# Optimization experiments

Measured on AMD Instinct MI355X. Metric: run time of the kernel, lower is better.

The kernel has to match this reference:

```python
import jax, jax.numpy as jnp
import numpy as np

N_GROUPS = 8
TOPK_GROUPS = 4
TOPK = 8
ROUTE_SCALE = 2.5

def setup_inputs() -> dict:
    key = jax.random.key(0)
    k1, k2, k3 = jax.random.split(key, 3)
    B, D, E = 8192, 7168, 256
    x = jax.random.normal(k1, (B, D), dtype=jnp.float32)
    weight = jax.random.normal(k2, (E, D), dtype=jnp.float32) / np.sqrt(D)
    bias = jax.random.normal(k3, (E,), dtype=jnp.float32) * 0.01
    return {"x": x, "weight": weight, "bias": bias}

def reference(x, weight, bias):
    B = x.shape[0]
    # linear scores: (B, E)
    scores = jnp.einsum('bd,ed->be', x, weight)
    # sigmoid score function
    s = jax.nn.sigmoid(scores)
    original_scores = s
    # bias correction for group selection (bias is not None since dim==7168)
    sb = s + bias
    # group view: (B, G, E/G)
    sg = sb.reshape(B, N_GROUPS, -1)
    # group score = sum of top-2 per group (bias branch)
    group_scores = jax.lax.top_k(sg, 2)[0].sum(axis=-1)  # (B, G)
    gidx = jax.lax.top_k(group_scores, TOPK_GROUPS)[1]   # (B, topk_groups)
    # boolean mask of selected groups
    gmask = jnp.zeros((B, N_GROUPS), dtype=bool).at[jnp.arange(B)[:, None], gidx].set(True)
    sg = jnp.where(gmask[:, :, None], sg, -jnp.inf)
    flat = sg.reshape(B, -1)  # (B, E)
    indices = jax.lax.top_k(flat, TOPK)[1]               # (B, topk)
    weights = jnp.take_along_axis(original_scores, indices, axis=1)
    # sigmoid path: normalize to sum 1, then scale
    weights = weights / weights.sum(axis=-1, keepdims=True)
    weights = weights * ROUTE_SCALE
    return weights.astype(x.dtype), indices
```

## Files before the change

kernel.cpp:

```cpp
#include <hip/hip_runtime.h>
#include <hip/hip_bf16.h>
#include <math.h>

#define DDIM 7168
#define NEXP 256
#define NGRP 8
#define TOPKG 4
#define TOPK 8
#define ROUTE_SCALE 2.5f

#define BM 128
#define BN 256
#define BK 32
#define KSPLIT 4
#define KPER (DDIM / KSPLIT)
#define NSTEP (KPER / BK)
#define NKTILE (DDIM / BK)
#define BT_ELEMS (NEXP * BK * 2)
#define AT_FLOATS (BM * BK)

typedef __attribute__((ext_vector_type(8))) short bf16x8;
typedef __attribute__((ext_vector_type(4))) float f32x4;
typedef unsigned int u32;
typedef unsigned short ushort_t;

static __device__ __forceinline__ ushort_t bf16_rne(float f) {
    u32 b = __float_as_uint(f);
    u32 r = (b + 0x7fffu + ((b >> 16) & 1u)) >> 16;
    return (ushort_t)r;
}
static __device__ __forceinline__ float bf16_to_f32(ushort_t h) {
    return __uint_as_float(((u32)h) << 16);
}
static __device__ __forceinline__ void split_elem(float f, short& h, short& l) {
    union { __hip_bfloat16 b; short s; } cv;
    cv.b = __float2bfloat16(f);
    h = cv.s;
    float hf = __uint_as_float(((u32)(ushort_t)cv.s) << 16);
    cv.b = __float2bfloat16(f - hf);
    l = cv.s;
}

__global__ __launch_bounds__(256) void wsplit_kernel(const float* __restrict__ w,
                                                     short* __restrict__ wsp)
{
    const int kt = blockIdx.x;
    const int e  = threadIdx.x;
    const float* wp = w + (size_t)e * DDIM + (size_t)kt * BK;
    short* tb = wsp + (size_t)kt * BT_ELEMS;
    const int fn = e >> 4, er = e & 15;
    #pragma unroll
    for (int jg = 0; jg < 4; jg++) {
        float f[8];
        *(float4*)&f[0] = *(const float4*)(wp + jg * 8);
        *(float4*)&f[4] = *(const float4*)(wp + jg * 8 + 4);
        ushort_t h[8], l[8];
        #pragma unroll
        for (int j = 0; j < 8; j++) {
            h[j] = bf16_rne(f[j]);
            l[j] = bf16_rne(f[j] - bf16_to_f32(h[j]));
        }
        const int lane = jg * 16 + er;
        *(uint4*)(tb + ((size_t)(0 * 16 + fn) * 64 + lane) * 8) = *(uint4*)h;
        *(uint4*)(tb + ((size_t)(1 * 16 + fn) * 64 + lane) * 8) = *(uint4*)l;
    }
}

__global__ __launch_bounds__(512, 2) void gemm_split_kernel(
    const float* __restrict__ x, const short* __restrict__ wsp,
    float* __restrict__ part, int Btok)
{
    __shared__ short Blds[3][BT_ELEMS];
    __shared__ float Alds[3][AT_FLOATS];

    const int bid  = blockIdx.x;
    const int xcd  = bid & 7;
    const int ksp  = xcd & 3;
    const int mt   = (bid >> 3) * 2 + (xcd >> 2);
    const int m0   = mt * BM;
    const int kbase = ksp * KPER;
    const int t    = threadIdx.x;
    const int wid  = t >> 6, lane = t & 63;
    const int wm   = wid >> 2, wn = wid & 3;
    const int lr   = lane & 15, lg = lane >> 4;

    const short* wt0 = wsp + (size_t)(ksp * NSTEP) * BT_ELEMS;

    const int arow0 = wid * 16 + (lane >> 3);
    const int akoff = 4 * ((lane & 7) ^ ((lane >> 3) & 7));
    const float* asrc0 = x + (size_t)(m0 + arow0) * DDIM + kbase + akoff;
    const size_t arow_step = (size_t)8 * DDIM;
    const int adst0 = wid * 2048 + lane * 16;

#define STAGE_B(stp, bptr) do {                                                            \
        const short* gt_ = wt0 + (size_t)(stp) * BT_ELEMS;                                 \
        _Pragma("unroll")                                                                  \
        for (int i_ = 0; i_ < 4; i_++) {                                                   \
            const int off_ = wid * 4096 + i_ * 1024;                                       \
            __builtin_amdgcn_global_load_lds(                                              \
                (const __attribute__((address_space(1))) u32*)((const char*)gt_ + off_ + lane * 16), \
                (__attribute__((address_space(3))) u32*)((char*)(bptr) + off_),            \
                16, 0, 0);                                                                 \
        } } while (0)

#define STAGE_A(stp, aptr) do {                                                            \
        _Pragma("unroll")                                                                  \
        for (int i_ = 0; i_ < 2; i_++) {                                                   \
            __builtin_amdgcn_global_load_lds(                                              \
                (const __attribute__((address_space(1))) u32*)(asrc0 + (size_t)i_ * arow_step + (size_t)(stp) * BK), \
                (__attribute__((address_space(3))) u32*)((char*)(aptr) + adst0 + i_ * 1024), \
                16, 0, 0);                                                                 \
        } } while (0)

    f32x4 acc[4][4];
    #pragma unroll
    for (int i = 0; i < 4; i++)
        #pragma unroll
        for (int j = 0; j < 4; j++) acc[i][j] = (f32x4){0.f, 0.f, 0.f, 0.f};

    short* pB_r = &Blds[0][0]; short* pB_1 = &Blds[1][0]; short* pB_2 = &Blds[2][0];
    float* pA_r = &Alds[0][0]; float* pA_1 = &Alds[1][0]; float* pA_2 = &Alds[2][0];

    STAGE_B(0, pB_r); STAGE_A(0, pA_r);
    STAGE_B(1, pB_1); STAGE_A(1, pA_1);

    for (int st = 0; st < NSTEP; st++) {
        if (st < NSTEP - 1) { asm volatile("s_waitcnt vmcnt(6)" ::: "memory"); }
        else                { asm volatile("s_waitcnt vmcnt(0)" ::: "memory"); }
        asm volatile("s_waitcnt lgkmcnt(0)" ::: "memory");
        __builtin_amdgcn_s_barrier();
        asm volatile("" ::: "memory");

        if (st + 2 < NSTEP) { STAGE_B(st + 2, pB_2); STAGE_A(st + 2, pA_2); }

        const char* ab = (const char*)pA_r;
        bf16x8 ah[4], al[4];
        #pragma unroll
        for (int fm = 0; fm < 4; fm++) {
            const int row = wm * 64 + fm * 16 + lr;
            const int rb  = row * 128;
            const int sw  = (lr & 7) << 4;
            float fr[8];
            *(float4*)&fr[0] = *(const float4*)(ab + rb + ((lg * 32) ^ sw));
            *(float4*)&fr[4] = *(const float4*)(ab + rb + ((lg * 32 + 16) ^ sw));
            union { bf16x8 v; short s[8]; } H, L;
            #pragma unroll
            for (int j = 0; j < 8; j++)
                split_elem(fr[j], H.s[j], L.s[j]);
            ah[fm] = H.v;
            al[fm] = L.v;
        }

        bf16x8 bhv[4], blv[4];
        #pragma unroll
        for (int fn = 0; fn < 4; fn++) {
            bhv[fn] = *(const bf16x8*)&pB_r[((size_t)(0 * 16 + wn * 4 + fn) * 64 + lane) * 8];
            blv[fn] = *(const bf16x8*)&pB_r[((size_t)(1 * 16 + wn * 4 + fn) * 64 + lane) * 8];
        }
        #pragma unroll
        for (int fn = 0; fn < 4; fn++)
            #pragma unroll
            for (int fm = 0; fm < 4; fm++)
                acc[fm][fn] = __builtin_amdgcn_mfma_f32_16x16x32_bf16(ah[fm], bhv[fn], acc[fm][fn], 0, 0, 0);
        #pragma unroll
        for (int fn = 0; fn < 4; fn++)
            #pragma unroll
            for (int fm = 0; fm < 4; fm++)
                acc[fm][fn] = __builtin_amdgcn_mfma_f32_16x16x32_bf16(ah[fm], blv[fn], acc[fm][fn], 0, 0, 0);
        #pragma unroll
        for (int fn = 0; fn < 4; fn++)
            #pragma unroll
            for (int fm = 0; fm < 4; fm++)
                acc[fm][fn] = __builtin_amdgcn_mfma_f32_16x16x32_bf16(al[fm], bhv[fn], acc[fm][fn], 0, 0, 0);

        { short* tb_ = pB_r; pB_r = pB_1; pB_1 = pB_2; pB_2 = tb_; }
        { float* ta_ = pA_r; pA_r = pA_1; pA_1 = pA_2; pA_2 = ta_; }
    }
#undef STAGE_B
#undef STAGE_A

    float* pp = part + (size_t)ksp * (size_t)Btok * NEXP;
    #pragma unroll
    for (int fm = 0; fm < 4; fm++) {
        const int row0 = m0 + wm * 64 + fm * 16 + lg * 4;
        #pragma unroll
        for (int fn = 0; fn < 4; fn++) {
            const int col = wn * 64 + fn * 16 + lr;
            #pragma unroll
            for (int rr = 0; rr < 4; rr++)
                pp[(size_t)(row0 + rr) * NEXP + col] = acc[fm][fn][rr];
        }
    }
}

__global__ __launch_bounds__(256) void gate_kernel(
    const float* __restrict__ part, const float* __restrict__ bias,
    float* __restrict__ out_w, float* __restrict__ out_i, int B)
{
    const int lane = threadIdx.x & 63;
    const int wid  = threadIdx.x >> 6;
    const int row  = blockIdx.x * 4 + wid;
    if (row >= B) return;

    const size_t plane = (size_t)B * NEXP;
    const float* pr = part + (size_t)row * NEXP + lane * 4;
    float4 v0 = *(const float4*)(pr);
    float4 v1 = *(const float4*)(pr + plane);
    float4 v2 = *(const float4*)(pr + 2 * plane);
    float4 v3 = *(const float4*)(pr + 3 * plane);
    float sc[4] = { v0.x + v1.x + v2.x + v3.x,
                    v0.y + v1.y + v2.y + v3.y,
                    v0.z + v1.z + v2.z + v3.z,
                    v0.w + v1.w + v2.w + v3.w };
    float4 bv = *(const float4*)(bias + lane * 4);
    const float bb[4] = { bv.x, bv.y, bv.z, bv.w };

    float so[4], sb[4];
    #pragma unroll
    for (int j = 0; j < 4; j++) {
        so[j] = 1.0f / (1.0f + expf(-sc[j]));
        sb[j] = so[j] + bb[j];
    }

    float m1 = sb[0], m2 = -INFINITY;
    #pragma unroll
    for (int j = 1; j < 4; j++) {
        if (sb[j] > m1)      { m2 = m1; m1 = sb[j]; }
        else if (sb[j] > m2) { m2 = sb[j]; }
    }
    #pragma unroll
    for (int m = 1; m <= 4; m <<= 1) {
        float o1 = __shfl_xor(m1, m);
        float o2 = __shfl_xor(m2, m);
        float hi = fmaxf(m1, o1);
        float lo = fminf(m1, o1);
        m1 = hi;
        m2 = fmaxf(lo, fmaxf(m2, o2));
    }
    float gscore = m1 + m2;
    int g = lane >> 3;

    float gs[NGRP];
    #pragma unroll
    for (int gg = 0; gg < NGRP; gg++) gs[gg] = __shfl(gscore, gg * 8);
    int rank = 0;
    #pragma unroll
    for (int gg = 0; gg < NGRP; gg++) {
        if (gg == g) continue;
        if (gs[gg] > gs[g] || (gs[gg] == gs[g] && gg < g)) rank++;
    }
    const bool selg = (rank < TOPKG);
    float mv[4];
    #pragma unroll
    for (int j = 0; j < 4; j++) mv[j] = selg ? sb[j] : -INFINITY;

    float wsel[TOPK];
    int   isel[TOPK];
    float wsum = 0.f;
    #pragma unroll
    for (int it = 0; it < TOPK; it++) {
        float v = mv[0]; int jj = 0;
        #pragma unroll
        for (int j = 1; j < 4; j++)
            if (mv[j] > v) { v = mv[j]; jj = j; }
        int gi = (lane << 2) | jj;
        #pragma unroll
        for (int m = 1; m < 64; m <<= 1) {
            float ov = __shfl_xor(v, m);
            int   oi = __shfl_xor(gi, m);
            if (ov > v || (ov == v && oi < gi)) { v = ov; gi = oi; }
        }
        int slot = gi & 3, src = gi >> 2;
        float cand = (slot == 0) ? so[0] : (slot == 1) ? so[1] : (slot == 2) ? so[2] : so[3];
        float sval = __shfl(cand, src);
        wsel[it] = sval; isel[it] = gi; wsum += sval;
        if (lane == src) mv[slot] = -INFINITY;
    }

    if (lane == 0) {
        float scl = ROUTE_SCALE / wsum;
        #pragma unroll
        for (int it = 0; it < TOPK; it++) {
            out_w[(size_t)row * TOPK + it] = wsel[it] * scl;
            out_i[(size_t)row * TOPK + it] = (float)isel[it];
        }
    }
}

extern "C" void kernel_launch(void* const* d_in, const int* in_sizes, int n_in,
                              void* d_out, int out_size, void* d_ws, size_t ws_size,
                              hipStream_t stream)
{
    const float* x    = (const float*)d_in[0];
    const float* w    = (const float*)d_in[1];
    const float* bias = (const float*)d_in[2];
    const int B = in_sizes[0] / DDIM;

    float* part = (float*)d_ws;
    short* wsp  = (short*)((char*)d_ws + (size_t)KSPLIT * B * NEXP * sizeof(float));

    float* out_w = (float*)d_out;
    float* out_i = out_w + (size_t)B * TOPK;

    hipLaunchKernelGGL(wsplit_kernel, dim3(NKTILE), dim3(256), 0, stream, w, wsp);
    hipLaunchKernelGGL(gemm_split_kernel, dim3((B / BM) * KSPLIT), dim3(512), 0, stream,
                       x, wsp, part, B);
    hipLaunchKernelGGL(gate_kernel, dim3((B + 3) / 4), dim3(256), 0, stream,
                       part, bias, out_w, out_i, B);
}
```

Baseline: 144.3 us.

## Split GEMM tile along experts into two 128-column halves with double buffering

The gemm block tile shrinks from 128x256 to 128x128, so each block covers half of the experts. The grid doubles and blocks drop from 512 to 256 threads. The pre-split weight layout is reorganized into per-half tiles, and the triple-buffered pipeline with manual waitcnt is replaced by a simpler double buffer using __syncthreads. This cuts LDS per block and raises block count, at the cost of loading each x tile twice (once per expert half) and a shallower prefetch pipeline.

Measured after the change: 141.4 us. 1.02x faster.

```diff
diff --git a/kernel.cpp b/kernel.cpp
--- a/kernel.cpp
+++ b/kernel.cpp
@@ -10,13 +10,13 @@
 #define ROUTE_SCALE 2.5f
 
 #define BM 128
-#define BN 256
+#define BN 128
 #define BK 32
 #define KSPLIT 4
 #define KPER (DDIM / KSPLIT)
 #define NSTEP (KPER / BK)
 #define NKTILE (DDIM / BK)
-#define BT_ELEMS (NEXP * BK * 2)
+#define BT_ELEMS (BN * BK * 2)
 #define AT_FLOATS (BM * BK)
 
 typedef __attribute__((ext_vector_type(8))) short bf16x8;
@@ -47,8 +47,8 @@
     const int kt = blockIdx.x;
     const int e  = threadIdx.x;
     const float* wp = w + (size_t)e * DDIM + (size_t)kt * BK;
-    short* tb = wsp + (size_t)kt * BT_ELEMS;
-    const int fn = e >> 4, er = e & 15;
+    const int nh = e >> 7, fn = (e >> 4) & 7, er = e & 15;
+    short* tb = wsp + ((size_t)kt * 2 + nh) * BT_ELEMS;
     #pragma unroll
     for (int jg = 0; jg < 4; jg++) {
         float f[8];
@@ -61,54 +61,55 @@
             l[j] = bf16_rne(f[j] - bf16_to_f32(h[j]));
         }
         const int lane = jg * 16 + er;
-        *(uint4*)(tb + ((size_t)(0 * 16 + fn) * 64 + lane) * 8) = *(uint4*)h;
-        *(uint4*)(tb + ((size_t)(1 * 16 + fn) * 64 + lane) * 8) = *(uint4*)l;
-    }
-}
-
-__global__ __launch_bounds__(512, 2) void gemm_split_kernel(
+        *(uint4*)(tb + ((size_t)(0 * 8 + fn) * 64 + lane) * 8) = *(uint4*)h;
+        *(uint4*)(tb + ((size_t)(1 * 8 + fn) * 64 + lane) * 8) = *(uint4*)l;
+    }
+}
+
+__global__ __launch_bounds__(256, 2) void gemm_split_kernel(
     const float* __restrict__ x, const short* __restrict__ wsp,
     float* __restrict__ part, int Btok)
 {
-    __shared__ short Blds[3][BT_ELEMS];
-    __shared__ float Alds[3][AT_FLOATS];
+    __shared__ short Blds[2][BT_ELEMS];
+    __shared__ float Alds[2][AT_FLOATS];
 
     const int bid  = blockIdx.x;
     const int xcd  = bid & 7;
     const int ksp  = xcd & 3;
-    const int mt   = (bid >> 3) * 2 + (xcd >> 2);
+    const int nh   = xcd >> 2;
+    const int mt   = bid >> 3;
     const int m0   = mt * BM;
     const int kbase = ksp * KPER;
     const int t    = threadIdx.x;
     const int wid  = t >> 6, lane = t & 63;
-    const int wm   = wid >> 2, wn = wid & 3;
+    const int wm   = wid >> 1, wn = wid & 1;
     const int lr   = lane & 15, lg = lane >> 4;
 
-    const short* wt0 = wsp + (size_t)(ksp * NSTEP) * BT_ELEMS;
-
-    const int arow0 = wid * 16 + (lane >> 3);
+    const short* wt0 = wsp + ((size_t)(ksp * NSTEP) * 2 + nh) * BT_ELEMS;
+
+    const int arow0 = wid * 32 + (lane >> 3);
     const int akoff = 4 * ((lane & 7) ^ ((lane >> 3) & 7));
     const float* asrc0 = x + (size_t)(m0 + arow0) * DDIM + kbase + akoff;
     const size_t arow_step = (size_t)8 * DDIM;
-    const int adst0 = wid * 2048 + lane * 16;
-
-#define STAGE_B(stp, bptr) do {                                                            \
-        const short* gt_ = wt0 + (size_t)(stp) * BT_ELEMS;                                 \
+    const int adst0 = wid * 4096 + lane * 16;
+
+#define STAGE_B(stp, buf) do {                                                             \
+        const short* gt_ = wt0 + (size_t)(stp) * 2 * BT_ELEMS;                             \
         _Pragma("unroll")                                                                  \
         for (int i_ = 0; i_ < 4; i_++) {                                                   \
             const int off_ = wid * 4096 + i_ * 1024;                                       \
             __builtin_amdgcn_global_load_lds(                                              \
                 (const __attribute__((address_space(1))) u32*)((const char*)gt_ + off_ + lane * 16), \
-                (__attribute__((address_space(3))) u32*)((char*)(bptr) + off_),            \
+                (__attribute__((address_space(3))) u32*)((char*)&Blds[buf][0] + off_),     \
                 16, 0, 0);                                                                 \
         } } while (0)
 
-#define STAGE_A(stp, aptr) do {                                                            \
+#define STAGE_A(stp, buf) do {                                                             \
         _Pragma("unroll")                                                                  \
-        for (int i_ = 0; i_ < 2; i_++) {                                                   \
+        for (int i_ = 0; i_ < 4; i_++) {                                                   \
             __builtin_amdgcn_global_load_lds(                                              \
                 (const __attribute__((address_space(1))) u32*)(asrc0 + (size_t)i_ * arow_step + (size_t)(stp) * BK), \
-                (__attribute__((address_space(3))) u32*)((char*)(aptr) + adst0 + i_ * 1024), \
+                (__attribute__((address_space(3))) u32*)((char*)&Alds[buf][0] + adst0 + i_ * 1024), \
                 16, 0, 0);                                                                 \
         } } while (0)
 
@@ -118,22 +119,19 @@
         #pragma unroll
         for (int j = 0; j < 4; j++) acc[i][j] = (f32x4){0.f, 0.f, 0.f, 0.f};
 
-    short* pB_r = &Blds[0][0]; short* pB_1 = &Blds[1][0]; short* pB_2 = &Blds[2][0];
-    float* pA_r = &Alds[0][0]; float* pA_1 = &Alds[1][0]; float* pA_2 = &Alds[2][0];
-
-    STAGE_B(0, pB_r); STAGE_A(0, pA_r);
-    STAGE_B(1, pB_1); STAGE_A(1, pA_1);
+    STAGE_B(0, 0);
+    STAGE_A(0, 0);
 
     for (int st = 0; st < NSTEP; st++) {
-        if (st < NSTEP - 1) { asm volatile("s_waitcnt vmcnt(6)" ::: "memory"); }
-        else                { asm volatile("s_waitcnt vmcnt(0)" ::: "memory"); }
-        asm volatile("s_waitcnt lgkmcnt(0)" ::: "memory");
-        __builtin_amdgcn_s_barrier();
-        asm volatile("" ::: "memory");
-
-        if (st + 2 < NSTEP) { STAGE_B(st + 2, pB_2); STAGE_A(st + 2, pA_2); }
-
-        const char* ab = (const char*)pA_r;
+        const int cur = st & 1;
+        __syncthreads();
+
+        if (st + 1 < NSTEP) {
+            STAGE_B(st + 1, cur ^ 1);
+            STAGE_A(st + 1, cur ^ 1);
+        }
+
+        const char* ab = (const char*)&Alds[cur][0];
         bf16x8 ah[4], al[4];
         #pragma unroll
         for (int fm = 0; fm < 4; fm++) {
@@ -154,8 +152,8 @@
         bf16x8 bhv[4], blv[4];
         #pragma unroll
         for (int fn = 0; fn < 4; fn++) {
-            bhv[fn] = *(const bf16x8*)&pB_r[((size_t)(0 * 16 + wn * 4 + fn) * 64 + lane) * 8];
-            blv[fn] = *(const bf16x8*)&pB_r[((size_t)(1 * 16 + wn * 4 + fn) * 64 + lane) * 8];
+            bhv[fn] = *(const bf16x8*)&Blds[cur][((size_t)(0 * 8 + wn * 4 + fn) * 64 + lane) * 8];
+            blv[fn] = *(const bf16x8*)&Blds[cur][((size_t)(1 * 8 + wn * 4 + fn) * 64 + lane) * 8];
         }
         #pragma unroll
         for (int fn = 0; fn < 4; fn++)
@@ -172,9 +170,6 @@
             #pragma unroll
             for (int fm = 0; fm < 4; fm++)
                 acc[fm][fn] = __builtin_amdgcn_mfma_f32_16x16x32_bf16(al[fm], bhv[fn], acc[fm][fn], 0, 0, 0);
-
-        { short* tb_ = pB_r; pB_r = pB_1; pB_1 = pB_2; pB_2 = tb_; }
-        { float* ta_ = pA_r; pA_r = pA_1; pA_1 = pA_2; pA_2 = ta_; }
     }
 #undef STAGE_B
 #undef STAGE_A
@@ -185,7 +180,7 @@
         const int row0 = m0 + wm * 64 + fm * 16 + lg * 4;
         #pragma unroll
         for (int fn = 0; fn < 4; fn++) {
-            const int col = wn * 64 + fn * 16 + lr;
+            const int col = nh * 128 + wn * 64 + fn * 16 + lr;
             #pragma unroll
             for (int rr = 0; rr < 4; rr++)
                 pp[(size_t)(row0 + rr) * NEXP + col] = acc[fm][fn][rr];
@@ -303,7 +298,7 @@
     float* out_i = out_w + (size_t)B * TOPK;
 
     hipLaunchKernelGGL(wsplit_kernel, dim3(NKTILE), dim3(256), 0, stream, w, wsp);
-    hipLaunchKernelGGL(gemm_split_kernel, dim3((B / BM) * KSPLIT), dim3(512), 0, stream,
+    hipLaunchKernelGGL(gemm_split_kernel, dim3((B / BM) * 2 * KSPLIT), dim3(256), 0, stream,
                        x, wsp, part, B);
     hipLaunchKernelGGL(gate_kernel, dim3((B + 3) / 4), dim3(256), 0, stream,
                        part, bias, out_w, out_i, B);
```
